# Kernel optimization log

Hardware: AMD Instinct MI355X
Metric: run time of the kernel (lower is better)

Reference implementation:

```python
import jax, jax.numpy as jnp
import numpy as np

# Config (matches init_kwargs)
HIDDEN = 1280
NUM_EXPERTS = 16
NUM_SHARED = 2
NUM_ROUTED = NUM_EXPERTS - NUM_SHARED          # 14
TOPK = 6 - NUM_SHARED                           # num_activated - num_shared = 4
INTERMED = int(int(HIDDEN * 4.0) * 0.25)        # 1280
B, S = 2, 2048


def setup_inputs() -> dict:
    key = jax.random.key(0)
    ks = jax.random.split(key, 12)
    sc = 0.02
    x = jax.random.normal(ks[0], (B, S, HIDDEN), dtype=jnp.float32)
    # shared experts, stacked over expert axis
    W1s = jax.random.normal(ks[1], (NUM_SHARED, HIDDEN, INTERMED), dtype=jnp.float32) * sc
    b1s = jnp.zeros((NUM_SHARED, INTERMED), dtype=jnp.float32)
    W2s = jax.random.normal(ks[2], (NUM_SHARED, INTERMED, HIDDEN), dtype=jnp.float32) * sc
    b2s = jnp.zeros((NUM_SHARED, HIDDEN), dtype=jnp.float32)
    # routed experts
    W1r = jax.random.normal(ks[3], (NUM_ROUTED, HIDDEN, INTERMED), dtype=jnp.float32) * sc
    b1r = jnp.zeros((NUM_ROUTED, INTERMED), dtype=jnp.float32)
    W2r = jax.random.normal(ks[4], (NUM_ROUTED, INTERMED, HIDDEN), dtype=jnp.float32) * sc
    b2r = jnp.zeros((NUM_ROUTED, HIDDEN), dtype=jnp.float32)
    # router
    Wr = jax.random.normal(ks[5], (HIDDEN, NUM_ROUTED), dtype=jnp.float32) * sc
    br = jnp.zeros((NUM_ROUTED,), dtype=jnp.float32)
    return {"x": x, "W1s": W1s, "b1s": b1s, "W2s": W2s, "b2s": b2s,
            "W1r": W1r, "b1r": b1r, "W2r": W2r, "b2r": b2r, "Wr": Wr, "br": br}


def _gelu(x):
    return jax.nn.gelu(x, approximate=False)  # torch nn.GELU default is exact erf


def reference(x, W1s, b1s, W2s, b2s, W1r, b1r, W2r, b2r, Wr, br):
    # shared experts: sum_e FFN_e(x)
    hs = _gelu(jnp.einsum('bsh,ehi->ebsi', x, W1s) + b1s[:, None, None, :])
    shared_out = jnp.einsum('ebsi,eih->bsh', hs, W2s) + b2s.sum(0)

    # router: softmax + top-k gates scattered back to dense [B,S,E]
    logits = jnp.einsum('bsh,he->bse', x, Wr) + br
    aff = jax.nn.softmax(logits, axis=-1)
    topk_vals, topk_idx = jax.lax.top_k(aff, TOPK)
    gates = (jax.nn.one_hot(topk_idx, NUM_ROUTED, dtype=aff.dtype)
             * topk_vals[..., None]).sum(axis=-2)  # [B,S,E]

    # naive dense dispatch: every routed expert over all tokens, gate-weighted
    hr = _gelu(jnp.einsum('bsh,ehi->ebsi', x, W1r) + b1r[:, None, None, :])
    expert_out = jnp.einsum('ebsi,eih->ebsh', hr, W2r) + b2r[:, None, None, :]
    routed_out = jnp.einsum('bse,ebsh->bsh', gates, expert_out)

    return shared_out + routed_out + x
```

## Files before the change

kernel.cpp:

```cpp
#include <hip/hip_runtime.h>
#include <hip/hip_bf16.h>
#include <math.h>

#define H      1280
#define NE     16
#define NR     14
#define TK     4
#define T      4096
#define NROWS  24576
#define MAXTILE 208

typedef __bf16 bf16x8 __attribute__((ext_vector_type(8)));
typedef float  f32x4  __attribute__((ext_vector_type(4)));

__device__ __forceinline__ unsigned short f2bf(float f) {
  unsigned int u = __float_as_uint(f);
  u += 0x7fffu + ((u >> 16) & 1u);
  return (unsigned short)(u >> 16);
}
__device__ __forceinline__ float bf2f(unsigned short u) {
  return __uint_as_float(((unsigned int)u) << 16);
}

__device__ __forceinline__ void gll16(const unsigned short* g, unsigned short* l) {
  __builtin_amdgcn_global_load_lds(
      (const __attribute__((address_space(1))) void*)g,
      (__attribute__((address_space(3))) void*)l, 16, 0, 0);
}

__global__ void k_init(int* cnt, int* fill) {
  int i = threadIdx.x;
  if (i < 16) { cnt[i] = 0; fill[i] = 0; }
}

__global__ void k_cast_x(const float* __restrict__ x, unsigned short* __restrict__ xb) {
  int i = blockIdx.x * 256 + threadIdx.x;
  float4 v = reinterpret_cast<const float4*>(x)[i];
  ushort4 b;
  b.x = f2bf(v.x); b.y = f2bf(v.y); b.z = f2bf(v.z); b.w = f2bf(v.w);
  reinterpret_cast<ushort4*>(xb)[i] = b;
}

__global__ void k_transpose(const float* __restrict__ W1s, const float* __restrict__ W2s,
                            const float* __restrict__ W1r, const float* __restrict__ W2r,
                            unsigned short* __restrict__ w1b, unsigned short* __restrict__ w2b) {
  int mat = blockIdx.z;
  int fam = mat >> 4;
  int e   = mat & 15;
  size_t msz = (size_t)H * H;
  const float* src;
  unsigned short* dst;
  if (fam == 0) {
    src = (e < 2) ? W1s + (size_t)e * msz : W1r + (size_t)(e - 2) * msz;
    dst = w1b + (size_t)e * msz;
  } else {
    src = (e < 2) ? W2s + (size_t)e * msz : W2r + (size_t)(e - 2) * msz;
    dst = w2b + (size_t)e * msz;
  }
  __shared__ unsigned short tile[64][68];
  int tx = threadIdx.x & 15;
  int ty = threadIdx.x >> 4;
  int bx = blockIdx.x * 64;
  int by = blockIdx.y * 64;
#pragma unroll
  for (int p = 0; p < 4; p++) {
    int r = p * 16 + ty;
    float4 v = *reinterpret_cast<const float4*>(&src[(size_t)(by + r) * H + bx + tx * 4]);
    tile[tx * 4 + 0][r] = f2bf(v.x);
    tile[tx * 4 + 1][r] = f2bf(v.y);
    tile[tx * 4 + 2][r] = f2bf(v.z);
    tile[tx * 4 + 3][r] = f2bf(v.w);
  }
  __syncthreads();
#pragma unroll
  for (int p = 0; p < 4; p++) {
    int n = p * 16 + ty;
    ushort4 o;
    o.x = tile[n][tx * 4 + 0];
    o.y = tile[n][tx * 4 + 1];
    o.z = tile[n][tx * 4 + 2];
    o.w = tile[n][tx * 4 + 3];
    *reinterpret_cast<ushort4*>(&dst[(size_t)(bx + n) * H + by + tx * 4]) = o;
  }
}

__global__ void k_router(const float* __restrict__ x, const float* __restrict__ Wr,
                         const float* __restrict__ br,
                         int* __restrict__ topk_e, float* __restrict__ topk_g) {
  int t  = blockIdx.x * 4 + (threadIdx.x >> 6);
  int ln = threadIdx.x & 63;
  float part[NR];
#pragma unroll
  for (int e = 0; e < NR; e++) part[e] = 0.f;
  const float* xr = x + (size_t)t * H;
  for (int k = ln; k < H; k += 64) {
    float xv = xr[k];
    const float* w = Wr + (size_t)k * NR;
#pragma unroll
    for (int e = 0; e < NR; e++) part[e] += xv * w[e];
  }
  float aff[NR];
#pragma unroll
  for (int e = 0; e < NR; e++) {
    float v = part[e];
#pragma unroll
    for (int off = 32; off; off >>= 1) v += __shfl_down(v, off);
    aff[e] = v + br[e];
  }
  if (ln == 0) {
    float mx = aff[0];
#pragma unroll
    for (int e = 1; e < NR; e++) mx = fmaxf(mx, aff[e]);
    float p[NR]; float s = 0.f;
#pragma unroll
    for (int e = 0; e < NR; e++) { p[e] = expf(aff[e] - mx); s += p[e]; }
    float inv = 1.f / s;
    unsigned used = 0;
    for (int j = 0; j < TK; j++) {
      int be = -1; float bv = -1.f;
#pragma unroll
      for (int e = 0; e < NR; e++)
        if (!((used >> e) & 1u) && p[e] > bv) { bv = p[e]; be = e; }
      used |= 1u << be;
      topk_e[t * TK + j] = be;
      topk_g[t * TK + j] = bv * inv;
    }
  }
}

__global__ void k_count(const int* __restrict__ topk_e, int* __restrict__ cnt) {
  __shared__ int hist[NR];
  int tid = threadIdx.x;
  if (tid < NR) hist[tid] = 0;
  __syncthreads();
  int t = blockIdx.x * 256 + tid;
#pragma unroll
  for (int j = 0; j < TK; j++)
    atomicAdd(&hist[topk_e[t * TK + j]], 1);
  __syncthreads();
  if (tid < NR) atomicAdd(&cnt[tid], hist[tid]);
}

__global__ void k_prefix(const int* __restrict__ cnt, int* __restrict__ segbase,
                         int* __restrict__ segcnt, int* __restrict__ tile_seg,
                         int* __restrict__ tile_m0) {
  if (threadIdx.x == 0) {
    int sc[NE];
    sc[0] = T; sc[1] = T;
    for (int e = 0; e < NR; e++) sc[2 + e] = cnt[e];
    int b = 0;
    for (int s = 0; s < NE; s++) { segbase[s] = b; segcnt[s] = sc[s]; b += sc[s]; }
    int nt = 0;
    for (int s = 0; s < NE; s++)
      for (int m = 0; m < sc[s]; m += 128) { tile_seg[nt] = s; tile_m0[nt] = m; nt++; }
    for (int i = nt; i < MAXTILE; i++) { tile_seg[i] = -1; tile_m0[i] = 0; }
  }
}

__global__ void k_fill(const int* __restrict__ topk_e,
                       const int* __restrict__ segbase, int* __restrict__ fill,
                       int* __restrict__ rowtok, int* __restrict__ tokrow) {
  __shared__ int lhist[NR];
  __shared__ int lbase[NR];
  int tid = threadIdx.x;
  if (tid < NR) lhist[tid] = 0;
  __syncthreads();
  int t = blockIdx.x * 256 + tid;
  rowtok[t]     = t;
  rowtok[T + t] = t;
  int e[TK], off[TK];
#pragma unroll
  for (int j = 0; j < TK; j++) {
    e[j]   = topk_e[t * TK + j];
    off[j] = atomicAdd(&lhist[e[j]], 1);
  }
  __syncthreads();
  if (tid < NR) lbase[tid] = atomicAdd(&fill[tid], lhist[tid]);
  __syncthreads();
#pragma unroll
  for (int j = 0; j < TK; j++) {
    int r = segbase[2 + e[j]] + lbase[e[j]] + off[j];
    rowtok[r] = t;
    tokrow[t * TK + j] = r;
  }
}


__global__ __launch_bounds__(256) void k_gemm1(
    const unsigned short* __restrict__ xb, const unsigned short* __restrict__ w1b,
    const float* __restrict__ b1s, const float* __restrict__ b1r,
    const int* __restrict__ rowtok, const int* __restrict__ segbase,
    const int* __restrict__ segcnt, const int* __restrict__ tile_seg,
    const int* __restrict__ tile_m0, unsigned short* __restrict__ hbuf) {
  int seg = tile_seg[blockIdx.y];
  if (seg < 0) return;
  int m0  = tile_m0[blockIdx.y];
  int cnt = segcnt[seg];
  int n0  = blockIdx.x * 128;
  int sb  = segbase[seg];
  const unsigned short* Bw = w1b + (size_t)seg * H * H;
  const float* bias = (seg < 2) ? b1s + (size_t)seg * H : b1r + (size_t)(seg - 2) * H;

  __shared__ __align__(16) unsigned short Al[128 * 64];
  __shared__ __align__(16) unsigned short Bl[128 * 64];

  int tid = threadIdx.x;
  int wv = tid >> 6, ln = tid & 63;
  int rw = (wv >> 1) * 64, cw = (wv & 1) * 64;
  int quad = ln >> 4, l16 = ln & 15;
  int lrow = tid >> 3;
  int ldst = (tid & 7) * 8;
  int lkc  = (((tid & 7) ^ (lrow & 7))) * 8;

  const unsigned short* asrc[4];
  const unsigned short* bsrc[4];
#pragma unroll
  for (int p = 0; p < 4; p++) {
    int row = p * 32 + lrow;
    int gm  = m0 + row;
    int tok = (gm < cnt) ? rowtok[sb + gm] : 0;
    asrc[p] = xb + (size_t)tok * H + lkc;
    bsrc[p] = Bw + (size_t)(n0 + row) * H + lkc;
  }

  int xsw = (quad ^ (l16 & 7)) * 8;

  f32x4 acc[4][4];
#pragma unroll
  for (int i = 0; i < 4; i++)
#pragma unroll
    for (int j = 0; j < 4; j++) acc[i][j] = (f32x4){0.f, 0.f, 0.f, 0.f};

  for (int k0 = 0; k0 < H; k0 += 64) {
    __syncthreads();
#pragma unroll
    for (int p = 0; p < 4; p++) {
      int row = p * 32 + lrow;
      gll16(asrc[p] + k0, &Al[row * 64 + ldst]);
      gll16(bsrc[p] + k0, &Bl[row * 64 + ldst]);
    }
    __syncthreads();
#pragma unroll
    for (int kk = 0; kk < 64; kk += 32) {
      bf16x8 af[4], bfr[4];
#pragma unroll
      for (int i = 0; i < 4; i++)
        af[i] = *reinterpret_cast<const bf16x8*>(&Al[(rw + i * 16 + l16) * 64 + (xsw ^ kk)]);
#pragma unroll
      for (int j = 0; j < 4; j++)
        bfr[j] = *reinterpret_cast<const bf16x8*>(&Bl[(cw + j * 16 + l16) * 64 + (xsw ^ kk)]);
#pragma unroll
      for (int i = 0; i < 4; i++)
#pragma unroll
        for (int j = 0; j < 4; j++)
          acc[i][j] = __builtin_amdgcn_mfma_f32_16x16x32_bf16(af[i], bfr[j], acc[i][j], 0, 0, 0);
    }
  }

#pragma unroll
  for (int i = 0; i < 4; i++) {
#pragma unroll
    for (int r = 0; r < 4; r++) {
      int m = m0 + rw + i * 16 + quad * 4 + r;
      if (m >= cnt) continue;
      size_t ro = (size_t)(sb + m) * H;
#pragma unroll
      for (int j = 0; j < 4; j++) {
        int n = n0 + cw + j * 16 + l16;
        float v = acc[i][j][r] + bias[n];
        float g = 0.5f * v * (1.f + erff(v * 0.70710678118654752f));
        hbuf[ro + n] = f2bf(g);
      }
    }
  }
}

__global__ __launch_bounds__(256) void k_gemm2(
    const unsigned short* __restrict__ hbuf, const unsigned short* __restrict__ w2b,
    const float* __restrict__ b2s, const float* __restrict__ b2r,
    const int* __restrict__ segbase, const int* __restrict__ segcnt,
    const int* __restrict__ tile_seg, const int* __restrict__ tile_m0,
    unsigned short* __restrict__ rbuf) {
  int seg = tile_seg[blockIdx.y];
  if (seg < 0) return;
  int m0  = tile_m0[blockIdx.y];
  int cnt = segcnt[seg];
  int n0  = blockIdx.x * 128;
  int sb  = segbase[seg];
  const unsigned short* Bw = w2b + (size_t)seg * H * H;
  const float* bias = (seg < 2) ? b2s + (size_t)seg * H : b2r + (size_t)(seg - 2) * H;

  __shared__ __align__(16) unsigned short Al[128 * 64];
  __shared__ __align__(16) unsigned short Bl[128 * 64];

  int tid = threadIdx.x;
  int wv = tid >> 6, ln = tid & 63;
  int rw = (wv >> 1) * 64, cw = (wv & 1) * 64;
  int quad = ln >> 4, l16 = ln & 15;
  int lrow = tid >> 3;
  int ldst = (tid & 7) * 8;
  int lkc  = (((tid & 7) ^ (lrow & 7))) * 8;

  const unsigned short* asrc[4];
  const unsigned short* bsrc[4];
#pragma unroll
  for (int p = 0; p < 4; p++) {
    int row = p * 32 + lrow;
    int ar  = sb + m0 + row;
    if (ar >= NROWS) ar = 0;
    asrc[p] = hbuf + (size_t)ar * H + lkc;
    bsrc[p] = Bw + (size_t)(n0 + row) * H + lkc;
  }

  int xsw = (quad ^ (l16 & 7)) * 8;

  f32x4 acc[4][4];
#pragma unroll
  for (int i = 0; i < 4; i++)
#pragma unroll
    for (int j = 0; j < 4; j++) acc[i][j] = (f32x4){0.f, 0.f, 0.f, 0.f};

  for (int k0 = 0; k0 < H; k0 += 64) {
    __syncthreads();
#pragma unroll
    for (int p = 0; p < 4; p++) {
      int row = p * 32 + lrow;
      gll16(asrc[p] + k0, &Al[row * 64 + ldst]);
      gll16(bsrc[p] + k0, &Bl[row * 64 + ldst]);
    }
    __syncthreads();
#pragma unroll
    for (int kk = 0; kk < 64; kk += 32) {
      bf16x8 af[4], bfr[4];
#pragma unroll
      for (int i = 0; i < 4; i++)
        af[i] = *reinterpret_cast<const bf16x8*>(&Al[(rw + i * 16 + l16) * 64 + (xsw ^ kk)]);
#pragma unroll
      for (int j = 0; j < 4; j++)
        bfr[j] = *reinterpret_cast<const bf16x8*>(&Bl[(cw + j * 16 + l16) * 64 + (xsw ^ kk)]);
#pragma unroll
      for (int i = 0; i < 4; i++)
#pragma unroll
        for (int j = 0; j < 4; j++)
          acc[i][j] = __builtin_amdgcn_mfma_f32_16x16x32_bf16(af[i], bfr[j], acc[i][j], 0, 0, 0);
    }
  }

#pragma unroll
  for (int i = 0; i < 4; i++) {
#pragma unroll
    for (int r = 0; r < 4; r++) {
      int m = m0 + rw + i * 16 + quad * 4 + r;
      if (m >= cnt) continue;
      size_t ro = (size_t)(sb + m) * H;
#pragma unroll
      for (int j = 0; j < 4; j++) {
        int n = n0 + cw + j * 16 + l16;
        rbuf[ro + n] = f2bf(acc[i][j][r] + bias[n]);
      }
    }
  }
}

__global__ void k_combine(const float* __restrict__ x, const unsigned short* __restrict__ rbuf,
                          const int* __restrict__ tokrow, const float* __restrict__ topk_g,
                          float* __restrict__ out) {
  int i = blockIdx.x * 256 + threadIdx.x;
  int t = i / (H / 4);
  int c = (i - t * (H / 4)) * 4;
  size_t xo = (size_t)t * H + c;
  float4 acc = *reinterpret_cast<const float4*>(&x[xo]);
  {
    ushort4 u0 = *reinterpret_cast<const ushort4*>(&rbuf[(size_t)t * H + c]);
    ushort4 u1 = *reinterpret_cast<const ushort4*>(&rbuf[(size_t)(T + t) * H + c]);
    acc.x += bf2f(u0.x) + bf2f(u1.x);
    acc.y += bf2f(u0.y) + bf2f(u1.y);
    acc.z += bf2f(u0.z) + bf2f(u1.z);
    acc.w += bf2f(u0.w) + bf2f(u1.w);
  }
#pragma unroll
  for (int j = 0; j < TK; j++) {
    int r   = tokrow[t * TK + j];
    float g = topk_g[t * TK + j];
    ushort4 u = *reinterpret_cast<const ushort4*>(&rbuf[(size_t)r * H + c]);
    acc.x += g * bf2f(u.x);
    acc.y += g * bf2f(u.y);
    acc.z += g * bf2f(u.z);
    acc.w += g * bf2f(u.w);
  }
  *reinterpret_cast<float4*>(&out[xo]) = acc;
}

extern "C" void kernel_launch(void* const* d_in, const int* in_sizes, int n_in,
                              void* d_out, int out_size, void* d_ws, size_t ws_size,
                              hipStream_t stream) {
  const float* x   = (const float*)d_in[0];
  const float* W1s = (const float*)d_in[1];
  const float* b1s = (const float*)d_in[2];
  const float* W2s = (const float*)d_in[3];
  const float* b2s = (const float*)d_in[4];
  const float* W1r = (const float*)d_in[5];
  const float* b1r = (const float*)d_in[6];
  const float* W2r = (const float*)d_in[7];
  const float* b2r = (const float*)d_in[8];
  const float* Wr  = (const float*)d_in[9];
  const float* br  = (const float*)d_in[10];
  float* out = (float*)d_out;

  char* ws = (char*)d_ws;
  const size_t SZ_XB = (size_t)T * H * 2;
  const size_t SZ_WB = (size_t)NE * H * H * 2;
  const size_t SZ_H  = (size_t)NROWS * H * 2;
  size_t off = 0;
  unsigned short* xb   = (unsigned short*)(ws + off); off += SZ_XB;
  unsigned short* w1b  = (unsigned short*)(ws + off); off += SZ_WB;
  unsigned short* w2b  = (unsigned short*)(ws + off); off += SZ_WB;
  unsigned short* hbuf = (unsigned short*)(ws + off); off += SZ_H;
  int*   rowtok  = (int*)(ws + off);   off += NROWS * 4;
  int*   tokrow  = (int*)(ws + off);   off += T * TK * 4;
  int*   topk_e  = (int*)(ws + off);   off += T * TK * 4;
  float* topk_g  = (float*)(ws + off); off += T * TK * 4;
  int*   cnt     = (int*)(ws + off);   off += 64;
  int*   fill    = (int*)(ws + off);   off += 64;
  int*   segbase = (int*)(ws + off);   off += 64;
  int*   segcnt  = (int*)(ws + off);   off += 64;
  int*   tile_seg = (int*)(ws + off);  off += MAXTILE * 4;
  int*   tile_m0  = (int*)(ws + off);  off += MAXTILE * 4;
  unsigned short* rbuf = (unsigned short*)ws;

  hipLaunchKernelGGL(k_init, dim3(1), dim3(64), 0, stream, cnt, fill);
  hipLaunchKernelGGL(k_cast_x, dim3((T * H / 4) / 256), dim3(256), 0, stream, x, xb);
  hipLaunchKernelGGL(k_transpose, dim3(20, 20, 32), dim3(256), 0, stream,
                     W1s, W2s, W1r, W2r, w1b, w2b);
  hipLaunchKernelGGL(k_router, dim3(T / 4), dim3(256), 0, stream, x, Wr, br, topk_e, topk_g);
  hipLaunchKernelGGL(k_count, dim3(T / 256), dim3(256), 0, stream, topk_e, cnt);
  hipLaunchKernelGGL(k_prefix, dim3(1), dim3(1), 0, stream, cnt, segbase, segcnt, tile_seg, tile_m0);
  hipLaunchKernelGGL(k_fill, dim3(T / 256), dim3(256), 0, stream,
                     topk_e, segbase, fill, rowtok, tokrow);
  hipLaunchKernelGGL(k_gemm1, dim3(10, MAXTILE, 1), dim3(256), 0, stream,
                     xb, w1b, b1s, b1r, rowtok, segbase, segcnt, tile_seg, tile_m0, hbuf);
  hipLaunchKernelGGL(k_gemm2, dim3(10, MAXTILE, 1), dim3(256), 0, stream,
                     hbuf, w2b, b2s, b2r, segbase, segcnt, tile_seg, tile_m0, rbuf);
  hipLaunchKernelGGL(k_combine, dim3((T * H / 4) / 256), dim3(256), 0, stream,
                     x, rbuf, tokrow, topk_g, out);
}
```

Before: 619.0 us.

## Enlarge grouped GEMM tiles to 256x256 with 512-thread blocks; vectorize transpose stores

Both expert GEMM kernels move from 128x128 tiles with 256 threads to 256x256 tiles with 512 threads, and each wave now computes a 128x64 sub-tile. The aim is more reuse of each loaded A and B tile and less global and LDS traffic per FLOP. The cost is 64KB of LDS per block, double the accumulator registers and more padding waste on partially filled expert segments. The tile list is rebuilt in 256-row steps, and the weight transpose now writes 16-byte vectors from a re-padded LDS tile.

```diff
diff --git a/kernel.cpp b/kernel.cpp
--- a/kernel.cpp
+++ b/kernel.cpp
@@ -8,10 +8,11 @@
 #define TK     4
 #define T      4096
 #define NROWS  24576
-#define MAXTILE 208
+#define MAXT   112
 
 typedef __bf16 bf16x8 __attribute__((ext_vector_type(8)));
 typedef float  f32x4  __attribute__((ext_vector_type(4)));
+typedef unsigned short us8 __attribute__((ext_vector_type(8)));
 
 __device__ __forceinline__ unsigned short f2bf(float f) {
   unsigned int u = __float_as_uint(f);
@@ -57,7 +58,7 @@
     src = (e < 2) ? W2s + (size_t)e * msz : W2r + (size_t)(e - 2) * msz;
     dst = w2b + (size_t)e * msz;
   }
-  __shared__ unsigned short tile[64][68];
+  __shared__ unsigned short tile[64][72];
   int tx = threadIdx.x & 15;
   int ty = threadIdx.x >> 4;
   int bx = blockIdx.x * 64;
@@ -72,15 +73,13 @@
     tile[tx * 4 + 3][r] = f2bf(v.w);
   }
   __syncthreads();
-#pragma unroll
-  for (int p = 0; p < 4; p++) {
-    int n = p * 16 + ty;
-    ushort4 o;
-    o.x = tile[n][tx * 4 + 0];
-    o.y = tile[n][tx * 4 + 1];
-    o.z = tile[n][tx * 4 + 2];
-    o.w = tile[n][tx * 4 + 3];
-    *reinterpret_cast<ushort4*>(&dst[(size_t)(bx + n) * H + by + tx * 4]) = o;
+  int tx8 = threadIdx.x & 7;
+  int rr  = threadIdx.x >> 3;
+#pragma unroll
+  for (int p = 0; p < 2; p++) {
+    int n = p * 32 + rr;
+    us8 o = *reinterpret_cast<const us8*>(&tile[n][tx8 * 8]);
+    *reinterpret_cast<us8*>(&dst[(size_t)(bx + n) * H + by + tx8 * 8]) = o;
   }
 }
 
@@ -152,8 +151,8 @@
     for (int s = 0; s < NE; s++) { segbase[s] = b; segcnt[s] = sc[s]; b += sc[s]; }
     int nt = 0;
     for (int s = 0; s < NE; s++)
-      for (int m = 0; m < sc[s]; m += 128) { tile_seg[nt] = s; tile_m0[nt] = m; nt++; }
-    for (int i = nt; i < MAXTILE; i++) { tile_seg[i] = -1; tile_m0[i] = 0; }
+      for (int m = 0; m < sc[s]; m += 256) { tile_seg[nt] = s; tile_m0[nt] = m; nt++; }
+    for (int i = nt; i < MAXT; i++) { tile_seg[i] = -1; tile_m0[i] = 0; }
   }
 }
 
@@ -186,7 +185,7 @@
 }
 
 
-__global__ __launch_bounds__(256) void k_gemm1(
+__global__ __launch_bounds__(512, 2) void k_gemm1(
     const unsigned short* __restrict__ xb, const unsigned short* __restrict__ w1b,
     const float* __restrict__ b1s, const float* __restrict__ b1r,
     const int* __restrict__ rowtok, const int* __restrict__ segbase,
@@ -196,17 +195,17 @@
   if (seg < 0) return;
   int m0  = tile_m0[blockIdx.y];
   int cnt = segcnt[seg];
-  int n0  = blockIdx.x * 128;
+  int n0  = blockIdx.x * 256;
   int sb  = segbase[seg];
   const unsigned short* Bw = w1b + (size_t)seg * H * H;
   const float* bias = (seg < 2) ? b1s + (size_t)seg * H : b1r + (size_t)(seg - 2) * H;
 
-  __shared__ __align__(16) unsigned short Al[128 * 64];
-  __shared__ __align__(16) unsigned short Bl[128 * 64];
+  __shared__ __align__(16) unsigned short Al[256 * 64];
+  __shared__ __align__(16) unsigned short Bl[256 * 64];
 
   int tid = threadIdx.x;
   int wv = tid >> 6, ln = tid & 63;
-  int rw = (wv >> 1) * 64, cw = (wv & 1) * 64;
+  int rw = (wv & 1) * 128, cw = (wv >> 1) * 64;
   int quad = ln >> 4, l16 = ln & 15;
   int lrow = tid >> 3;
   int ldst = (tid & 7) * 8;
@@ -216,7 +215,7 @@
   const unsigned short* bsrc[4];
 #pragma unroll
   for (int p = 0; p < 4; p++) {
-    int row = p * 32 + lrow;
+    int row = p * 64 + lrow;
     int gm  = m0 + row;
     int tok = (gm < cnt) ? rowtok[sb + gm] : 0;
     asrc[p] = xb + (size_t)tok * H + lkc;
@@ -225,9 +224,9 @@
 
   int xsw = (quad ^ (l16 & 7)) * 8;
 
-  f32x4 acc[4][4];
-#pragma unroll
-  for (int i = 0; i < 4; i++)
+  f32x4 acc[8][4];
+#pragma unroll
+  for (int i = 0; i < 8; i++)
 #pragma unroll
     for (int j = 0; j < 4; j++) acc[i][j] = (f32x4){0.f, 0.f, 0.f, 0.f};
 
@@ -235,22 +234,22 @@
     __syncthreads();
 #pragma unroll
     for (int p = 0; p < 4; p++) {
-      int row = p * 32 + lrow;
+      int row = p * 64 + lrow;
       gll16(asrc[p] + k0, &Al[row * 64 + ldst]);
       gll16(bsrc[p] + k0, &Bl[row * 64 + ldst]);
     }
     __syncthreads();
 #pragma unroll
     for (int kk = 0; kk < 64; kk += 32) {
-      bf16x8 af[4], bfr[4];
-#pragma unroll
-      for (int i = 0; i < 4; i++)
+      bf16x8 af[8], bfr[4];
+#pragma unroll
+      for (int i = 0; i < 8; i++)
         af[i] = *reinterpret_cast<const bf16x8*>(&Al[(rw + i * 16 + l16) * 64 + (xsw ^ kk)]);
 #pragma unroll
       for (int j = 0; j < 4; j++)
         bfr[j] = *reinterpret_cast<const bf16x8*>(&Bl[(cw + j * 16 + l16) * 64 + (xsw ^ kk)]);
 #pragma unroll
-      for (int i = 0; i < 4; i++)
+      for (int i = 0; i < 8; i++)
 #pragma unroll
         for (int j = 0; j < 4; j++)
           acc[i][j] = __builtin_amdgcn_mfma_f32_16x16x32_bf16(af[i], bfr[j], acc[i][j], 0, 0, 0);
@@ -258,7 +257,7 @@
   }
 
 #pragma unroll
-  for (int i = 0; i < 4; i++) {
+  for (int i = 0; i < 8; i++) {
 #pragma unroll
     for (int r = 0; r < 4; r++) {
       int m = m0 + rw + i * 16 + quad * 4 + r;
@@ -275,7 +274,7 @@
   }
 }
 
-__global__ __launch_bounds__(256) void k_gemm2(
+__global__ __launch_bounds__(512, 2) void k_gemm2(
     const unsigned short* __restrict__ hbuf, const unsigned short* __restrict__ w2b,
     const float* __restrict__ b2s, const float* __restrict__ b2r,
     const int* __restrict__ segbase, const int* __restrict__ segcnt,
@@ -285,17 +284,17 @@
   if (seg < 0) return;
   int m0  = tile_m0[blockIdx.y];
   int cnt = segcnt[seg];
-  int n0  = blockIdx.x * 128;
+  int n0  = blockIdx.x * 256;
   int sb  = segbase[seg];
   const unsigned short* Bw = w2b + (size_t)seg * H * H;
   const float* bias = (seg < 2) ? b2s + (size_t)seg * H : b2r + (size_t)(seg - 2) * H;
 
-  __shared__ __align__(16) unsigned short Al[128 * 64];
-  __shared__ __align__(16) unsigned short Bl[128 * 64];
+  __shared__ __align__(16) unsigned short Al[256 * 64];
+  __shared__ __align__(16) unsigned short Bl[256 * 64];
 
   int tid = threadIdx.x;
   int wv = tid >> 6, ln = tid & 63;
-  int rw = (wv >> 1) * 64, cw = (wv & 1) * 64;
+  int rw = (wv & 1) * 128, cw = (wv >> 1) * 64;
   int quad = ln >> 4, l16 = ln & 15;
   int lrow = tid >> 3;
   int ldst = (tid & 7) * 8;
@@ -305,7 +304,7 @@
   const unsigned short* bsrc[4];
 #pragma unroll
   for (int p = 0; p < 4; p++) {
-    int row = p * 32 + lrow;
+    int row = p * 64 + lrow;
     int ar  = sb + m0 + row;
     if (ar >= NROWS) ar = 0;
     asrc[p] = hbuf + (size_t)ar * H + lkc;
@@ -314,9 +313,9 @@
 
   int xsw = (quad ^ (l16 & 7)) * 8;
 
-  f32x4 acc[4][4];
-#pragma unroll
-  for (int i = 0; i < 4; i++)
+  f32x4 acc[8][4];
+#pragma unroll
+  for (int i = 0; i < 8; i++)
 #pragma unroll
     for (int j = 0; j < 4; j++) acc[i][j] = (f32x4){0.f, 0.f, 0.f, 0.f};
 
@@ -324,22 +323,22 @@
     __syncthreads();
 #pragma unroll
     for (int p = 0; p < 4; p++) {
-      int row = p * 32 + lrow;
+      int row = p * 64 + lrow;
       gll16(asrc[p] + k0, &Al[row * 64 + ldst]);
       gll16(bsrc[p] + k0, &Bl[row * 64 + ldst]);
     }
     __syncthreads();
 #pragma unroll
     for (int kk = 0; kk < 64; kk += 32) {
-      bf16x8 af[4], bfr[4];
-#pragma unroll
-      for (int i = 0; i < 4; i++)
+      bf16x8 af[8], bfr[4];
+#pragma unroll
+      for (int i = 0; i < 8; i++)
         af[i] = *reinterpret_cast<const bf16x8*>(&Al[(rw + i * 16 + l16) * 64 + (xsw ^ kk)]);
 #pragma unroll
       for (int j = 0; j < 4; j++)
         bfr[j] = *reinterpret_cast<const bf16x8*>(&Bl[(cw + j * 16 + l16) * 64 + (xsw ^ kk)]);
 #pragma unroll
-      for (int i = 0; i < 4; i++)
+      for (int i = 0; i < 8; i++)
 #pragma unroll
         for (int j = 0; j < 4; j++)
           acc[i][j] = __builtin_amdgcn_mfma_f32_16x16x32_bf16(af[i], bfr[j], acc[i][j], 0, 0, 0);
@@ -347,7 +346,7 @@
   }
 
 #pragma unroll
-  for (int i = 0; i < 4; i++) {
+  for (int i = 0; i < 8; i++) {
 #pragma unroll
     for (int r = 0; r < 4; r++) {
       int m = m0 + rw + i * 16 + quad * 4 + r;
@@ -424,8 +423,8 @@
   int*   fill    = (int*)(ws + off);   off += 64;
   int*   segbase = (int*)(ws + off);   off += 64;
   int*   segcnt  = (int*)(ws + off);   off += 64;
-  int*   tile_seg = (int*)(ws + off);  off += MAXTILE * 4;
-  int*   tile_m0  = (int*)(ws + off);  off += MAXTILE * 4;
+  int*   tile_seg = (int*)(ws + off);  off += MAXT * 4;
+  int*   tile_m0  = (int*)(ws + off);  off += MAXT * 4;
   unsigned short* rbuf = (unsigned short*)ws;
 
   hipLaunchKernelGGL(k_init, dim3(1), dim3(64), 0, stream, cnt, fill);
@@ -437,9 +436,9 @@
   hipLaunchKernelGGL(k_prefix, dim3(1), dim3(1), 0, stream, cnt, segbase, segcnt, tile_seg, tile_m0);
   hipLaunchKernelGGL(k_fill, dim3(T / 256), dim3(256), 0, stream,
                      topk_e, segbase, fill, rowtok, tokrow);
-  hipLaunchKernelGGL(k_gemm1, dim3(10, MAXTILE, 1), dim3(256), 0, stream,
+  hipLaunchKernelGGL(k_gemm1, dim3(5, MAXT, 1), dim3(512), 0, stream,
                      xb, w1b, b1s, b1r, rowtok, segbase, segcnt, tile_seg, tile_m0, hbuf);
-  hipLaunchKernelGGL(k_gemm2, dim3(10, MAXTILE, 1), dim3(256), 0, stream,
+  hipLaunchKernelGGL(k_gemm2, dim3(5, MAXT, 1), dim3(512), 0, stream,
                      hbuf, w2b, b2s, b2r, segbase, segcnt, tile_seg, tile_m0, rbuf);
   hipLaunchKernelGGL(k_combine, dim3((T * H / 4) / 256), dim3(256), 0, stream,
                      x, rbuf, tokrow, topk_g, out);
```

New measurement: 611.0 us. About the same (-1.3%).
